# Kernel tuning notes

Hardware: AMD Instinct MI355X
Metric: run time of the kernel (lower is better)

The kernel has to match this reference:

```python
import jax, jax.numpy as jnp
import numpy as np

DEPTH = 8  # remaining_depth at the root
N_INTERNAL = 2**DEPTH - 1  # 255, level-order indexed
N_LEAF = 2**DEPTH          # 256
CLAMP_MIN = 1e-5


def setup_inputs() -> dict:
    key = jax.random.key(0)
    k1, k2, k3 = jax.random.split(key, 3)
    B, D_in, D_out = 65536, 1024, 128
    x = jax.random.normal(k1, (B, D_in), dtype=jnp.float32)
    # one independent Linear(D_in,1) per internal node (deepcopy of split_function),
    # packed into a single [D_in, N_INTERNAL] matrix, level-order
    W_split = jax.random.normal(k2, (D_in, N_INTERNAL), dtype=jnp.float32) * (1.0 / np.sqrt(D_in))
    b_split = jnp.zeros((N_INTERNAL,), dtype=jnp.float32)
    # leaf values: uniform(-a, a) with a = sqrt(6/output_dim), per the torch init
    a = (6.0 / D_out) ** 0.5
    leaf_values = jax.random.uniform(k3, (N_LEAF, D_out), minval=-a, maxval=a, dtype=jnp.float32)
    return {"x": x, "W_split": W_split, "b_split": b_split, "leaf_values": leaf_values}


def reference(x, W_split, b_split, leaf_values):
    B = x.shape[0]
    # gate probability of every internal node in one batched GEMM: [B, N_INTERNAL]
    P = jax.nn.sigmoid(x @ W_split + b_split)
    # accumulate soft routing probability to each leaf, level by level
    probs = jnp.ones((B, 1), dtype=x.dtype)
    for d in range(DEPTH):
        p = P[:, 2**d - 1 : 2**(d + 1) - 1]  # gates at level d: [B, 2^d]
        # child order: left = (1-p), right = p (matches recursion ordering)
        probs = jnp.stack([(1.0 - p) * probs, p * probs], axis=-1).reshape(B, 2**(d + 1))
    out = probs @ leaf_values  # [B, D_out]: sum_leaf path_prob * value
    # regularization: sum over internal nodes of -0.5 * 2^-depth * mean_b log(clamp(p(1-p)))
    weights = jnp.concatenate(
        [jnp.full((2**d,), 2.0 ** (-d), dtype=x.dtype) for d in range(DEPTH)]
    )  # [N_INTERNAL]
    reg = jnp.sum(-0.5 * weights * jnp.mean(jnp.log(jnp.maximum(P * (1.0 - P), CLAMP_MIN)), axis=0))
    return out, reg
```

## Files before the change

### kernel.cpp

```cpp
#include <hip/hip_runtime.h>

#define B_TOT   65536
#define DIN     1024
#define NNODES  255
#define NPAD    256
#define DOUT    128
#define BM      128
#define BK      64
#define NKT     (DIN / BK)

typedef __attribute__((ext_vector_type(8))) _Float16      f16x8;
typedef __attribute__((ext_vector_type(4))) float         f32x4;
typedef __attribute__((ext_vector_type(4))) unsigned short u16x4;
typedef __attribute__((ext_vector_type(8))) unsigned short u16x8;
typedef unsigned short u16;
typedef unsigned int   u32;

__device__ __forceinline__ u16 f2h(float f) {
  _Float16 h = (_Float16)f;
  return __builtin_bit_cast(u16, h);
}
__device__ __forceinline__ float h2f(u16 b) {
  return (float)__builtin_bit_cast(_Float16, b);
}
__device__ __forceinline__ u32 pk2h(float a, float b) {
  return __builtin_bit_cast(u32, __builtin_amdgcn_cvt_pkrtz(a, b));
}

__device__ __forceinline__ int swz64(int row, int col) {
  return (row << 6) + ((((col >> 3) ^ row) & 7) << 3) + (col & 7);
}
__device__ __forceinline__ int swzP(int row, int col) {
  int g = col >> 3;
  int gs = (g & ~7) | ((g ^ row) & 7);
  return (row << 8) + (gs << 3) + (col & 7);
}

__global__ void prep_w(const float* __restrict__ Wsp, u16* __restrict__ WtG) {
  __shared__ float t[64][65];
  const int tid = threadIdx.x;
  const int wn = blockIdx.x;
  const int kc = blockIdx.y;
  const int bn = wn * 64, bk = kc * 64;
  {
    int n = tid & 63, kr0 = tid >> 6;
    #pragma unroll
    for (int i = 0; i < 16; ++i) {
      int k = kr0 + i * 4;
      int node = bn + n;
      t[k][n] = (node < NNODES) ? Wsp[(size_t)(bk + k) * NNODES + node] : 0.0f;
    }
  }
  __syncthreads();
  #pragma unroll
  for (int half = 0; half < 2; ++half) {
    int f = half * 256 + tid;
    int nt = f >> 7, rem = f & 127;
    int ks = rem >> 6, rem2 = rem & 63;
    int quad = rem2 >> 4, l15 = rem2 & 15;
    int nl = nt * 16 + l15;
    u16x8 v;
    #pragma unroll
    for (int j = 0; j < 8; ++j)
      v[j] = f2h(t[ks * 32 + quad * 8 + j][nl]);
    size_t F = (size_t)((((kc * 4 + wn) * 4 + nt) * 2 + ks) * 64 + (quad * 16 + l15));
    *(u16x8*)&WtG[F * 8] = v;
  }
}

__global__ void prep_leaf(const float* __restrict__ leaf, u16* __restrict__ lT) {
  int t = blockIdx.x * 256 + threadIdx.x;
  int j = t & 127, l = t >> 7;
  lT[j * NPAD + l] = f2h(leaf[l * DOUT + j]);
}

__global__ void finalize(const float* __restrict__ pw, float* __restrict__ regp) {
  int t = threadIdx.x;
  float s = 0.0f;
  #pragma unroll
  for (int i = 0; i < 8; ++i) s += pw[i * 512 + t];
  #pragma unroll
  for (int off = 32; off > 0; off >>= 1) s += __shfl_down(s, off, 64);
  __shared__ float red[8];
  if ((t & 63) == 0) red[t >> 6] = s;
  __syncthreads();
  if (t == 0) {
    float tot = 0.0f;
    #pragma unroll
    for (int i = 0; i < 8; ++i) tot += red[i];
    *regp = tot * (-0.5f / 65536.0f);
  }
}

__global__ __launch_bounds__(512, 4) void fused_sdt(
    const float* __restrict__ x, const float* __restrict__ bsp,
    const u16* __restrict__ WtG, const u16* __restrict__ lT,
    float* __restrict__ out, float* __restrict__ pw)
{
  __shared__ char smem[65536] __attribute__((aligned(16)));
  u16* xs0 = (u16*)smem;
  u16* xs1 = xs0 + 8192;
  u16* PB  = (u16*)smem;

  const int tid  = threadIdx.x;
  const int lane = tid & 63;
  const int w    = tid >> 6;
  const int l15  = lane & 15;
  const int quad = lane >> 4;
  const int wm   = w >> 2;
  const int wn   = w & 3;
  const int blk  = blockIdx.x;

  const float* xg = x + (size_t)blk * BM * DIN;

  f32x4 acc[4][4];
  #pragma unroll
  for (int mt = 0; mt < 4; ++mt)
    #pragma unroll
    for (int nt = 0; nt < 4; ++nt) {
      f32x4 z = {0.0f, 0.0f, 0.0f, 0.0f};
      acc[mt][nt] = z;
    }

  {
    #pragma unroll
    for (int i = 0; i < 4; ++i) {
      int idx = i * 512 + tid;
      int row = idx >> 4, kg = idx & 15;
      float4 v = *(const float4*)(xg + (size_t)row * DIN + kg * 4);
      u32 lo = pk2h(v.x, v.y);
      u32 hi = pk2h(v.z, v.w);
      u16x4 h;
      h.x = lo & 0xffff; h.y = lo >> 16;
      h.z = hi & 0xffff; h.w = hi >> 16;
      *(u16x4*)&xs0[swz64(row, kg * 4)] = h;
    }
  }
  __syncthreads();

  u16* xcur = xs0;
  u16* xnxt = xs1;
  for (int kc = 0; kc < NKT; ++kc) {
    float4 xv[4];
    const bool pf = (kc + 1 < NKT);
    if (pf) {
      #pragma unroll
      for (int i = 0; i < 4; ++i) {
        int idx = i * 512 + tid;
        int row = idx >> 4, kg = idx & 15;
        xv[i] = *(const float4*)(xg + (size_t)row * DIN + (kc + 1) * BK + kg * 4);
      }
    }
    const u16* wbase = WtG + (size_t)kc * 16384 + (size_t)wn * 4096;
    __builtin_amdgcn_s_setprio(1);
    #pragma unroll
    for (int ks = 0; ks < 2; ++ks) {
      const int kk = ks * 32 + quad * 8;
      f16x8 A[4], Bf[4];
      #pragma unroll
      for (int nt = 0; nt < 4; ++nt)
        Bf[nt] = *(const f16x8*)&wbase[nt * 1024 + ks * 512 + lane * 8];
      #pragma unroll
      for (int mt = 0; mt < 4; ++mt)
        A[mt] = *(const f16x8*)&xcur[swz64(wm * 64 + mt * 16 + l15, kk)];
      #pragma unroll
      for (int mt = 0; mt < 4; ++mt)
        #pragma unroll
        for (int nt = 0; nt < 4; ++nt)
          acc[mt][nt] = __builtin_amdgcn_mfma_f32_16x16x32_f16(
              A[mt], Bf[nt], acc[mt][nt], 0, 0, 0);
    }
    __builtin_amdgcn_s_setprio(0);
    if (pf) {
      #pragma unroll
      for (int i = 0; i < 4; ++i) {
        int idx = i * 512 + tid;
        int row = idx >> 4, kg = idx & 15;
        u32 lo = pk2h(xv[i].x, xv[i].y);
        u32 hi = pk2h(xv[i].z, xv[i].w);
        u16x4 h;
        h.x = lo & 0xffff; h.y = lo >> 16;
        h.z = hi & 0xffff; h.w = hi >> 16;
        *(u16x4*)&xnxt[swz64(row, kg * 4)] = h;
      }
    }
    __syncthreads();
    u16* tsw = xcur; xcur = xnxt; xnxt = tsw;
  }

  float rsum = 0.0f;
  float bv[4];
  #pragma unroll
  for (int nt = 0; nt < 4; ++nt) {
    int c = wn * 64 + nt * 16 + l15;
    bv[nt] = (c < NNODES) ? bsp[c] : 0.0f;
  }
  #pragma unroll
  for (int mt = 0; mt < 4; ++mt) {
    #pragma unroll
    for (int nt = 0; nt < 4; ++nt) {
      int c = wn * 64 + nt * 16 + l15;
      #pragma unroll
      for (int r = 0; r < 4; ++r) {
        int row = wm * 64 + mt * 16 + quad * 4 + r;
        float z = acc[mt][nt][r] + bv[nt];
        float e = __expf(-z);
        float p = __builtin_amdgcn_rcpf(1.0f + e);
        PB[swzP(row, c)] = f2h(p);
        if (c < NNODES) {
          float v = fmaxf(p * (1.0f - p), 1e-5f);
          int d = 31 - __clz(c + 1);
          float wgt = __builtin_bit_cast(float, (u32)(127 - d) << 23);
          rsum += wgt * __logf(v);
        }
      }
    }
  }
  #pragma unroll
  for (int off = 32; off > 0; off >>= 1) rsum += __shfl_down(rsum, off, 64);
  if (lane == 0) pw[blk * 8 + w] = rsum;
  __syncthreads();

  for (int rr = 0; rr < 16; ++rr) {
    int row = (w << 4) + rr;
    float prod = 1.0f;
    #pragma unroll
    for (int d = 0; d < 6; ++d) {
      int node = (1 << d) - 1 + (lane >> (6 - d));
      float pv = h2f(PB[swzP(row, node)]);
      prod *= ((lane >> (5 - d)) & 1) ? pv : (1.0f - pv);
    }
    float p6  = h2f(PB[swzP(row, 63 + lane)]);
    float p7a = h2f(PB[swzP(row, 127 + 2 * lane)]);
    float p7b = h2f(PB[swzP(row, 128 + 2 * lane)]);
    float a0 = prod * (1.0f - p6), a1 = prod * p6;
    u16x4 o;
    o.x = f2h(a0 * (1.0f - p7a));
    o.y = f2h(a0 * p7a);
    o.z = f2h(a1 * (1.0f - p7b));
    o.w = f2h(a1 * p7b);
    *(u16x4*)&PB[swzP(row, 4 * lane)] = o;
  }
  __syncthreads();

  f32x4 acc2[4][2];
  #pragma unroll
  for (int mt = 0; mt < 4; ++mt)
    #pragma unroll
    for (int nt = 0; nt < 2; ++nt) {
      f32x4 z = {0.0f, 0.0f, 0.0f, 0.0f};
      acc2[mt][nt] = z;
    }
  for (int kc = 0; kc < 4; ++kc) {
    #pragma unroll
    for (int ks = 0; ks < 2; ++ks) {
      const int kk = kc * 64 + ks * 32 + quad * 8;
      f16x8 Af[4], Bf2[2];
      #pragma unroll
      for (int nt = 0; nt < 2; ++nt)
        Bf2[nt] = *(const f16x8*)&lT[(wn * 32 + nt * 16 + l15) * NPAD + kk];
      #pragma unroll
      for (int mt = 0; mt < 4; ++mt)
        Af[mt] = *(const f16x8*)&PB[swzP(wm * 64 + mt * 16 + l15, kk)];
      #pragma unroll
      for (int mt = 0; mt < 4; ++mt)
        #pragma unroll
        for (int nt = 0; nt < 2; ++nt)
          acc2[mt][nt] = __builtin_amdgcn_mfma_f32_16x16x32_f16(
              Af[mt], Bf2[nt], acc2[mt][nt], 0, 0, 0);
    }
  }
  #pragma unroll
  for (int mt = 0; mt < 4; ++mt)
    #pragma unroll
    for (int nt = 0; nt < 2; ++nt)
      #pragma unroll
      for (int r = 0; r < 4; ++r) {
        int row = wm * 64 + mt * 16 + quad * 4 + r;
        int col = wn * 32 + nt * 16 + l15;
        out[(size_t)(blk * BM + row) * DOUT + col] = acc2[mt][nt][r];
      }
}

extern "C" void kernel_launch(void* const* d_in, const int* in_sizes, int n_in,
                              void* d_out, int out_size, void* d_ws, size_t ws_size,
                              hipStream_t stream) {
  (void)in_sizes; (void)n_in; (void)out_size; (void)ws_size;
  const float* x    = (const float*)d_in[0];
  const float* Wsp  = (const float*)d_in[1];
  const float* bsp  = (const float*)d_in[2];
  const float* leaf = (const float*)d_in[3];
  float* out  = (float*)d_out;
  float* regp = out + (size_t)B_TOT * DOUT;

  u16* WtG = (u16*)d_ws;
  u16* lT  = WtG + NPAD * DIN;
  float* pw = (float*)(lT + NPAD * DOUT);

  prep_w<<<dim3(4, 16), 256, 0, stream>>>(Wsp, WtG);
  prep_leaf<<<(NPAD * DOUT) / 256, 256, 0, stream>>>(leaf, lT);
  fused_sdt<<<B_TOT / BM, 512, 0, stream>>>(x, bsp, WtG, lT, out, pw);
  finalize<<<1, 512, 0, stream>>>(pw, regp);
}
```

Baseline: 437.2 us.

## Stage x tiles via direct global-to-LDS fp32 loads, convert to fp16 at fragment read

New measurement: 422.5 us. -3.3%, faster.

```diff
diff --git a/kernel.cpp b/kernel.cpp
--- a/kernel.cpp
+++ b/kernel.cpp
@@ -13,6 +13,7 @@
 typedef __attribute__((ext_vector_type(4))) float         f32x4;
 typedef __attribute__((ext_vector_type(4))) unsigned short u16x4;
 typedef __attribute__((ext_vector_type(8))) unsigned short u16x8;
+typedef __attribute__((ext_vector_type(4))) unsigned int   u32x4;
 typedef unsigned short u16;
 typedef unsigned int   u32;
 
@@ -26,10 +27,12 @@
 __device__ __forceinline__ u32 pk2h(float a, float b) {
   return __builtin_bit_cast(u32, __builtin_amdgcn_cvt_pkrtz(a, b));
 }
-
-__device__ __forceinline__ int swz64(int row, int col) {
-  return (row << 6) + ((((col >> 3) ^ row) & 7) << 3) + (col & 7);
-}
+__device__ __forceinline__ void cp16_g2s(const float* g, float* l) {
+  __builtin_amdgcn_global_load_lds(
+      (const __attribute__((address_space(1))) unsigned int*)g,
+      (__attribute__((address_space(3))) unsigned int*)l, 16, 0, 0);
+}
+
 __device__ __forceinline__ int swzP(int row, int col) {
   int g = col >> 3;
   int gs = (g & ~7) | ((g ^ row) & 7);
@@ -98,9 +101,9 @@
     float* __restrict__ out, float* __restrict__ pw)
 {
   __shared__ char smem[65536] __attribute__((aligned(16)));
-  u16* xs0 = (u16*)smem;
-  u16* xs1 = xs0 + 8192;
-  u16* PB  = (u16*)smem;
+  float* xs0 = (float*)smem;
+  float* xs1 = xs0 + 8192;
+  u16*   PB  = (u16*)smem;
 
   const int tid  = threadIdx.x;
   const int lane = tid & 63;
@@ -122,70 +125,56 @@
       acc[mt][nt] = z;
     }
 
-  {
+  auto stage_x = [&](float* buf, int kt) {
     #pragma unroll
     for (int i = 0; i < 4; ++i) {
-      int idx = i * 512 + tid;
-      int row = idx >> 4, kg = idx & 15;
-      float4 v = *(const float4*)(xg + (size_t)row * DIN + kg * 4);
-      u32 lo = pk2h(v.x, v.y);
-      u32 hi = pk2h(v.z, v.w);
-      u16x4 h;
-      h.x = lo & 0xffff; h.y = lo >> 16;
-      h.z = hi & 0xffff; h.w = hi >> 16;
-      *(u16x4*)&xs0[swz64(row, kg * 4)] = h;
-    }
-  }
-  __syncthreads();
-
-  u16* xcur = xs0;
-  u16* xnxt = xs1;
+      int s   = (w * 4 + i) * 64 + lane;
+      int row = s >> 4;
+      int g   = ((s & 15) ^ row) & 15;
+      cp16_g2s(xg + (size_t)row * DIN + kt * BK + g * 4,
+               buf + (w * 4 + i) * 256);
+    }
+  };
+
+  stage_x(xs0, 0);
+  __syncthreads();
+
+  float* xcur = xs0;
+  float* xnxt = xs1;
   for (int kc = 0; kc < NKT; ++kc) {
-    float4 xv[4];
-    const bool pf = (kc + 1 < NKT);
-    if (pf) {
-      #pragma unroll
-      for (int i = 0; i < 4; ++i) {
-        int idx = i * 512 + tid;
-        int row = idx >> 4, kg = idx & 15;
-        xv[i] = *(const float4*)(xg + (size_t)row * DIN + (kc + 1) * BK + kg * 4);
-      }
-    }
-    const u16* wbase = WtG + (size_t)kc * 16384 + (size_t)wn * 4096;
+    f16x8 Bf[8];
+    {
+      const u16* wbase = WtG + (size_t)kc * 16384 + (size_t)wn * 4096;
+      #pragma unroll
+      for (int q = 0; q < 8; ++q)
+        Bf[q] = *(const f16x8*)&wbase[(q & 3) * 1024 + (q >> 2) * 512 + lane * 8];
+    }
+    if (kc + 1 < NKT) stage_x(xnxt, kc + 1);
     __builtin_amdgcn_s_setprio(1);
     #pragma unroll
     for (int ks = 0; ks < 2; ++ks) {
-      const int kk = ks * 32 + quad * 8;
-      f16x8 A[4], Bf[4];
-      #pragma unroll
-      for (int nt = 0; nt < 4; ++nt)
-        Bf[nt] = *(const f16x8*)&wbase[nt * 1024 + ks * 512 + lane * 8];
-      #pragma unroll
-      for (int mt = 0; mt < 4; ++mt)
-        A[mt] = *(const f16x8*)&xcur[swz64(wm * 64 + mt * 16 + l15, kk)];
-      #pragma unroll
-      for (int mt = 0; mt < 4; ++mt)
+      const int g0 = ks * 8 + quad * 2;
+      #pragma unroll
+      for (int mt = 0; mt < 4; ++mt) {
+        const int row = wm * 64 + mt * 16 + l15;
+        const float* rb = xcur + row * 64;
+        f32x4 lo = *(const f32x4*)(rb + (((g0    ) ^ row) & 15) * 4);
+        f32x4 hi = *(const f32x4*)(rb + (((g0 + 1) ^ row) & 15) * 4);
+        u32x4 aw;
+        aw[0] = pk2h(lo[0], lo[1]);
+        aw[1] = pk2h(lo[2], lo[3]);
+        aw[2] = pk2h(hi[0], hi[1]);
+        aw[3] = pk2h(hi[2], hi[3]);
+        f16x8 A = __builtin_bit_cast(f16x8, aw);
         #pragma unroll
         for (int nt = 0; nt < 4; ++nt)
           acc[mt][nt] = __builtin_amdgcn_mfma_f32_16x16x32_f16(
-              A[mt], Bf[nt], acc[mt][nt], 0, 0, 0);
+              A, Bf[ks * 4 + nt], acc[mt][nt], 0, 0, 0);
+      }
     }
     __builtin_amdgcn_s_setprio(0);
-    if (pf) {
-      #pragma unroll
-      for (int i = 0; i < 4; ++i) {
-        int idx = i * 512 + tid;
-        int row = idx >> 4, kg = idx & 15;
-        u32 lo = pk2h(xv[i].x, xv[i].y);
-        u32 hi = pk2h(xv[i].z, xv[i].w);
-        u16x4 h;
-        h.x = lo & 0xffff; h.y = lo >> 16;
-        h.z = hi & 0xffff; h.w = hi >> 16;
-        *(u16x4*)&xnxt[swz64(row, kg * 4)] = h;
-      }
-    }
     __syncthreads();
-    u16* tsw = xcur; xcur = xnxt; xnxt = tsw;
+    float* tsw = xcur; xcur = xnxt; xnxt = tsw;
   }
 
   float rsum = 0.0f;
```
